# Optimization experiments

Measured on AMD Instinct MI355X. Metric: run time of the kernel, lower is better.

## Reference

```python
import jax, jax.numpy as jnp
import numpy as np

B, T, IN = 8, 1000, 80
CONV = 256
CCEP = 222            # ltv_out_channels
FFT_SIZE = 1024
HOP = 256
WIN = 2 * HOP         # 512
PAD = (FFT_SIZE - CCEP) // 2   # 401
NFFT = 2048


def _conv1d_same(x, W, b, groups):
    # x: (B,T,C); W: (O, C//groups, 3); equivalent to torch Conv1d pad=2 then [1:-1]
    y = jax.lax.conv_general_dilated(
        jnp.transpose(x, (0, 2, 1)), W, (1,), [(1, 1)],
        feature_group_count=groups,
        dimension_numbers=('NCH', 'OIH', 'NCH'))
    return jnp.transpose(y, (0, 2, 1)) + b


def _forward(x, z, W1, b1, W2, b2, W3, b3, W4, b4):
    Bx, Tx, _ = x.shape
    # ---- ConvLayers ----
    h = jax.nn.relu(_conv1d_same(x, W1, b1, 1))
    h = jax.nn.relu(_conv1d_same(h, W2, b2, 8))
    h = jax.nn.relu(_conv1d_same(h, W3, b3, 8))
    ccep = _conv1d_same(h, W4, b4, 1)            # (B,T,222)
    q = jnp.arange(1, CCEP // 2 + 1, dtype=x.dtype)
    quef = jnp.concatenate([q[::-1], q])          # [111..1,1..111]
    ccep = ccep / quef
    # ---- ccep -> impulse (log-magnitude cepstrum -> minimum-ish phase impulse) ----
    c = jnp.pad(ccep, ((0, 0), (0, 0), (PAD, PAD)))           # (B,T,1024)
    Y = jnp.fft.fft(c, n=FFT_SIZE, axis=-1)
    mag = jnp.power(10.0, Y.real)
    imp = jnp.fft.ifft(mag * jnp.exp(1j * Y.imag), n=FFT_SIZE, axis=-1).real  # (B,T,1024)
    # ---- time-varying impulse convolution (cross-correlation per frame) ----
    L = z.shape[-1]
    zz = z.reshape(Bx, 1, L)
    zp = jnp.pad(zz, ((0, 0), (0, 0), (WIN // 2 - 1, WIN // 2)))
    starts = jnp.arange(Tx) * HOP
    frames = zp[:, :, starts[:, None] + jnp.arange(WIN)]       # (B,1,T,512)
    fp = jnp.pad(frames, ((0, 0), (0, 0), (0, 0), (FFT_SIZE // 2 - 1, FFT_SIZE // 2)))  # len 1535
    # corr[s] = sum_k fp[s+k] * imp[k], s in [0,512); linear corr via zero-padded FFT
    Fz = jnp.fft.rfft(fp, n=NFFT, axis=-1)                     # (B,1,T,NFFT//2+1)
    Fy = jnp.fft.rfft(imp, n=NFFT, axis=-1)[:, None]           # (B,1,T,NFFT//2+1)
    corr = jnp.fft.irfft(Fz * jnp.conj(Fy), n=NFFT, axis=-1)[..., :WIN]  # (B,1,T,512)
    # ---- overlap-add ----
    n = jnp.arange(WIN, dtype=x.dtype)
    win = 0.5 * (1.0 - jnp.cos(2.0 * jnp.pi * n / WIN))        # periodic hann, win_norm=1
    zw = corr * win
    l, r = zw[..., :HOP], zw[..., HOP:]
    out = l + jnp.roll(r, 1, axis=2)
    return out.reshape(Bx, 1, Tx * HOP)


def setup_inputs() -> dict:
    key = jax.random.key(0)
    ks = jax.random.split(key, 12)
    x = jax.random.normal(ks[0], (B, T, IN), dtype=jnp.float32)
    z = jax.random.normal(ks[1], (B, 1, T * HOP), dtype=jnp.float32)
    def w(k, o, i, kk, scale):
        return jax.random.normal(k, (o, i, kk), dtype=jnp.float32) * (scale / np.sqrt(i * kk))
    W1 = w(ks[2], CONV, IN, 3, 1.0)
    b1 = jnp.zeros((CONV,), jnp.float32)
    W2 = w(ks[3], CONV, CONV // 8, 3, 1.0)
    b2 = jnp.zeros((CONV,), jnp.float32)
    W3 = w(ks[4], CONV, CONV // 8, 3, 1.0)
    b3 = jnp.zeros((CONV,), jnp.float32)
    W4 = w(ks[5], CCEP, CONV, 3, 0.01)   # small scale keeps 10**(.) well-conditioned
    b4 = jnp.zeros((CCEP,), jnp.float32)
    return {"x": x, "z": z, "W1": W1, "b1": b1, "W2": W2, "b2": b2,
            "W3": W3, "b3": b3, "W4": W4, "b4": b4}


def reference(x, z, W1, b1, W2, b2, W3, b3, W4, b4):
    return _forward(x, z, W1, b1, W2, b2, W3, b3, W4, b4)
```

## Files before the change

kernel.cpp:

```cpp
#include <hip/hip_runtime.h>
#include <hip/hip_bf16.h>

#define T_LEN 1000
#define B_N 8
#define IN_CH 80
#define CONV_CH 256
#define CCEP_N 222

typedef short s8v __attribute__((ext_vector_type(8)));
typedef float f16v __attribute__((ext_vector_type(16)));

#define TWO_PI 6.28318530717958647692f

__global__ __launch_bounds__(256) void k_prep(
    const float* __restrict__ W1, const float* __restrict__ W2,
    const float* __restrict__ W3, const float* __restrict__ W4,
    float* __restrict__ Wt1, float* __restrict__ Wt2, float* __restrict__ Wt3,
    __hip_bfloat16* __restrict__ Wc, float2* __restrict__ twTab,
    float* __restrict__ winTab) {
  const int bid = blockIdx.x, tid = threadIdx.x;
  if (bid < 240) {
    int e = bid * 256 + tid;
    int o = e / 240, k = e - o * 240;
    Wt1[k * 256 + o] = W1[e];
  } else if (bid < 336) {
    int e = (bid - 240) * 256 + tid;
    int o = e / 96, k = e - o * 96;
    Wt2[k * 256 + o] = W2[e];
  } else if (bid < 432) {
    int e = (bid - 336) * 256 + tid;
    int o = e / 96, k = e - o * 96;
    Wt3[k * 256 + o] = W3[e];
  } else if (bid < 1200) {
    int e = (bid - 432) * 256 + tid;
    int kloc = e & 31, n = (e >> 5) & 255, chg = e >> 13;
    int kp = chg * 32 + kloc;
    int kappa = kp >> 8, i = kp & 255;
    float v = 0.f;
    if (n < CCEP_N) {
      float invq = 1.f / (float)((n < 111) ? (111 - n) : (n - 110));
      v = W4[n * 768 + i * 3 + kappa] * invq;
    }
    Wc[e] = __float2bfloat16(v);
  } else {
    int e = (bid - 1200) * 256 + tid;
    if (e < 1020) {
      int Q, off;
      if (e < 768)       { Q = 256; off = 0; }
      else if (e < 960)  { Q = 64;  off = 768; }
      else if (e < 1008) { Q = 16;  off = 960; }
      else               { Q = 4;   off = 1008; }
      int rem = e - off;
      int r = rem / Q, pos = rem - r * Q;
      float ang = (TWO_PI * (float)((r + 1) * pos)) / (float)(4 * Q);
      float s, c;
      sincosf(ang, &s, &c);
      twTab[e] = make_float2(c, s);
    } else if (e < 1532) {
      int n = e - 1020;
      winTab[n] = (0.5f - 0.5f * cosf(TWO_PI * (float)n / 512.f)) * (1.f / 1024.f);
    }
  }
}

__global__ __launch_bounds__(256) void k_conv1t(const float* __restrict__ x,
    const float* __restrict__ Wt, const float* __restrict__ bias,
    float* __restrict__ out) {
  const int b = blockIdx.y;
  const int t0 = blockIdx.x * 10;
  const int o = threadIdx.x;
  __shared__ float hs[IN_CH * 14];
  for (int e = threadIdx.x; e < 12 * IN_CH; e += 256) {
    int r = e / IN_CH, c = e - r * IN_CH;
    int t = t0 - 1 + r;
    hs[c * 14 + r] = (t >= 0 && t < T_LEN) ? x[(b * T_LEN + t) * IN_CH + c] : 0.f;
  }
  __syncthreads();
  float acc[10];
  float bv = bias[o];
#pragma unroll
  for (int j = 0; j < 10; j++) acc[j] = bv;
  for (int i = 0; i < IN_CH; i++) {
    float w0 = Wt[(3 * i + 0) * 256 + o];
    float w1 = Wt[(3 * i + 1) * 256 + o];
    float w2 = Wt[(3 * i + 2) * 256 + o];
    const float* row = &hs[i * 14];
    float a[12];
#pragma unroll
    for (int u = 0; u < 6; u++) *(float2*)&a[2 * u] = *(const float2*)(row + 2 * u);
#pragma unroll
    for (int j = 0; j < 10; j++) {
      acc[j] = fmaf(a[j], w0, acc[j]);
      acc[j] = fmaf(a[j + 1], w1, acc[j]);
      acc[j] = fmaf(a[j + 2], w2, acc[j]);
    }
  }
#pragma unroll
  for (int j = 0; j < 10; j++)
    out[(b * T_LEN + t0 + j) * CONV_CH + o] = fmaxf(acc[j], 0.f);
}

__global__ __launch_bounds__(256) void k_convgt(const float* __restrict__ h,
    const float* __restrict__ Wt, const float* __restrict__ bias,
    float* __restrict__ out) {
  const int b = blockIdx.y;
  const int t0 = blockIdx.x * 10;
  const int o = threadIdx.x;
  const int cb = (o >> 5) << 5;
  __shared__ float hs[CONV_CH * 14];
  for (int e = threadIdx.x; e < 12 * CONV_CH; e += 256) {
    int r = e >> 8, c = e & 255;
    int t = t0 - 1 + r;
    hs[c * 14 + r] = (t >= 0 && t < T_LEN) ? h[(b * T_LEN + t) * CONV_CH + c] : 0.f;
  }
  __syncthreads();
  float acc[10];
  float bv = bias[o];
#pragma unroll
  for (int j = 0; j < 10; j++) acc[j] = bv;
  for (int i = 0; i < 32; i++) {
    float w0 = Wt[(3 * i + 0) * 256 + o];
    float w1 = Wt[(3 * i + 1) * 256 + o];
    float w2 = Wt[(3 * i + 2) * 256 + o];
    const float* row = &hs[(cb + i) * 14];
    float a[12];
#pragma unroll
    for (int u = 0; u < 6; u++) *(float2*)&a[2 * u] = *(const float2*)(row + 2 * u);
#pragma unroll
    for (int j = 0; j < 10; j++) {
      acc[j] = fmaf(a[j], w0, acc[j]);
      acc[j] = fmaf(a[j + 1], w1, acc[j]);
      acc[j] = fmaf(a[j + 2], w2, acc[j]);
    }
  }
#pragma unroll
  for (int j = 0; j < 10; j++)
    out[(b * T_LEN + t0 + j) * CONV_CH + o] = fmaxf(acc[j], 0.f);
}

__global__ __launch_bounds__(256) void k_convgt_b(const float* __restrict__ h,
    const float* __restrict__ Wt, const float* __restrict__ bias,
    __hip_bfloat16* __restrict__ out) {
  const int b = blockIdx.y;
  const int t0 = blockIdx.x * 10;
  const int o = threadIdx.x;
  const int cb = (o >> 5) << 5;
  __shared__ float hs[CONV_CH * 14];
  for (int e = threadIdx.x; e < 12 * CONV_CH; e += 256) {
    int r = e >> 8, c = e & 255;
    int t = t0 - 1 + r;
    hs[c * 14 + r] = (t >= 0 && t < T_LEN) ? h[(b * T_LEN + t) * CONV_CH + c] : 0.f;
  }
  __syncthreads();
  float acc[10];
  float bv = bias[o];
#pragma unroll
  for (int j = 0; j < 10; j++) acc[j] = bv;
  for (int i = 0; i < 32; i++) {
    float w0 = Wt[(3 * i + 0) * 256 + o];
    float w1 = Wt[(3 * i + 1) * 256 + o];
    float w2 = Wt[(3 * i + 2) * 256 + o];
    const float* row = &hs[(cb + i) * 14];
    float a[12];
#pragma unroll
    for (int u = 0; u < 6; u++) *(float2*)&a[2 * u] = *(const float2*)(row + 2 * u);
#pragma unroll
    for (int j = 0; j < 10; j++) {
      acc[j] = fmaf(a[j], w0, acc[j]);
      acc[j] = fmaf(a[j + 1], w1, acc[j]);
      acc[j] = fmaf(a[j + 2], w2, acc[j]);
    }
  }
#pragma unroll
  for (int j = 0; j < 10; j++)
    out[(b * T_LEN + t0 + j) * CONV_CH + o] = __float2bfloat16(fmaxf(acc[j], 0.f));
}

#define APITCH 264
#define BPITCH 40
#define PSTRIDE 1792000
__global__ __launch_bounds__(256) void k_conv4m(
    const __hip_bfloat16* __restrict__ h3, const __hip_bfloat16* __restrict__ Wc,
    const float* __restrict__ bias, float* __restrict__ Pbase) {
  const int mb = blockIdx.x, b = blockIdx.y, ks = blockIdx.z;
  float* __restrict__ P = Pbase + (size_t)ks * PSTRIDE;
  const int t0 = mb * 64;
  const int tid = threadIdx.x;
  const int w = tid >> 6, lane = tid & 63;
  const int wm = w >> 1, wn = w & 1;
  const int lm = lane & 31, half = lane >> 5;

  __shared__ short h3s[67 * APITCH];
  __shared__ short Bs[2][256 * BPITCH];

  const ushort* h3u = (const ushort*)h3;
  for (int g = tid; g < 67 * 64; g += 256) {
    int rr = g >> 6, c4 = g & 63;
    int t = t0 + rr - 1;
    uint2 v = make_uint2(0u, 0u);
    if (t >= 0 && t < T_LEN)
      v = *(const uint2*)(h3u + (b * T_LEN + t) * CONV_CH + c4 * 4);
    *(uint2*)(h3s + rr * APITCH + c4 * 4) = v;
  }

  const ushort* Wu = (const ushort*)(Wc) + (size_t)(ks * 6) * 8192;
#pragma unroll
  for (int it = 0; it < 4; ++it) {
    int idx = (it * 256 + tid) * 8;
    uint4 v = *(const uint4*)(Wu + idx);
    int n = idx >> 5, kloc = idx & 31;
    *(uint4*)(Bs[0] + n * BPITCH + kloc) = v;
  }
  __syncthreads();

  f16v acc0 = {}, acc1 = {}, acc2 = {}, acc3 = {};

  for (int ch = 0; ch < 6; ++ch) {
    const int p = ch & 1;
    if (ch < 5) {
      const ushort* src = Wu + (ch + 1) * 8192;
#pragma unroll
      for (int it = 0; it < 4; ++it) {
        int idx = (it * 256 + tid) * 8;
        uint4 v = *(const uint4*)(src + idx);
        int n = idx >> 5, kloc = idx & 31;
        *(uint4*)(Bs[p ^ 1] + n * BPITCH + kloc) = v;
      }
    }
#pragma unroll
    for (int s = 0; s < 2; ++s) {
      int k0 = ks * 192 + ch * 32 + s * 16;
      int kappa = k0 >> 8, i0 = k0 & 255;
      s8v a = *(const s8v*)(h3s + (wm * 32 + lm + kappa) * APITCH + i0 + half * 8);
      const short* bp = Bs[p] + (wn * 128 + lm) * BPITCH + s * 16 + half * 8;
      s8v b0 = *(const s8v*)(bp);
      s8v b1 = *(const s8v*)(bp + 32 * BPITCH);
      s8v b2 = *(const s8v*)(bp + 64 * BPITCH);
      s8v b3 = *(const s8v*)(bp + 96 * BPITCH);
      acc0 = __builtin_amdgcn_mfma_f32_32x32x16_bf16(a, b0, acc0, 0, 0, 0);
      acc1 = __builtin_amdgcn_mfma_f32_32x32x16_bf16(a, b1, acc1, 0, 0, 0);
      acc2 = __builtin_amdgcn_mfma_f32_32x32x16_bf16(a, b2, acc2, 0, 0, 0);
      acc3 = __builtin_amdgcn_mfma_f32_32x32x16_bf16(a, b3, acc3, 0, 0, 0);
    }
    __syncthreads();
  }

  const int col = lm;
#pragma unroll
  for (int nt = 0; nt < 4; ++nt) {
    int c = wn * 128 + nt * 32 + col;
    if (c >= CCEP_N) continue;
    float bq = 0.f;
    if (ks == 0) {
      float invq = 1.f / (float)((c < 111) ? (111 - c) : (c - 110));
      bq = bias[c] * invq;
    }
    const f16v* A = (nt == 0) ? &acc0 : (nt == 1) ? &acc1 : (nt == 2) ? &acc2 : &acc3;
#pragma unroll
    for (int reg = 0; reg < 16; ++reg) {
      int row = (reg & 3) + 8 * (reg >> 2) + 4 * half;
      int t = t0 + wm * 32 + row;
      if (t < T_LEN)
        P[(size_t)(b * T_LEN + t) * 224 + c] = (*A)[reg] + bq;
    }
  }
}

__device__ __forceinline__ float2 cmul(float2 a, float2 b) {
  return make_float2(fmaf(a.x, b.x, -(a.y * b.y)), fmaf(a.x, b.y, a.y * b.x));
}
__device__ __forceinline__ float2 cadd(float2 a, float2 b) { return make_float2(a.x + b.x, a.y + b.y); }
__device__ __forceinline__ float2 csub(float2 a, float2 b) { return make_float2(a.x - b.x, a.y - b.y); }

#define LIDX(i) ((i) + ((i) >> 2))

template <int Q, int OFF>
__device__ __forceinline__ void fwd_stage_t(float2* __restrict__ X,
    const float2* __restrict__ Tw, int j) {
  const int pos = j & (Q - 1);
  const int base = ((j - pos) << 2) + pos;
  float2 e1 = Tw[OFF + pos], e2 = Tw[OFF + Q + pos], e3 = Tw[OFF + 2 * Q + pos];
  const float2 w1 = make_float2(e1.x, -e1.y);
  const float2 w2 = make_float2(e2.x, -e2.y);
  const float2 w3 = make_float2(e3.x, -e3.y);
  float2 a = X[LIDX(base)], b = X[LIDX(base + Q)];
  float2 cc = X[LIDX(base + 2 * Q)], d = X[LIDX(base + 3 * Q)];
  float2 t0 = cadd(a, cc), t1 = csub(a, cc), t2 = cadd(b, d), bd = csub(b, d);
  float2 t3 = make_float2(bd.y, -bd.x);
  X[LIDX(base)]         = cadd(t0, t2);
  X[LIDX(base + Q)]     = cmul(cadd(t1, t3), w1);
  X[LIDX(base + 2 * Q)] = cmul(csub(t0, t2), w2);
  X[LIDX(base + 3 * Q)] = cmul(csub(t1, t3), w3);
}

template <int Q, int OFF>
__device__ __forceinline__ void inv_stage_t(float2* __restrict__ X,
    const float2* __restrict__ Tw, int j) {
  const int pos = j & (Q - 1);
  const int base = ((j - pos) << 2) + pos;
  const float2 w1 = Tw[OFF + pos];
  const float2 w2 = Tw[OFF + Q + pos];
  const float2 w3 = Tw[OFF + 2 * Q + pos];
  float2 a = X[LIDX(base)];
  float2 b = cmul(X[LIDX(base + Q)], w1);
  float2 cc = cmul(X[LIDX(base + 2 * Q)], w2);
  float2 d = cmul(X[LIDX(base + 3 * Q)], w3);
  float2 t0 = cadd(a, cc), t1 = csub(a, cc), t2 = cadd(b, d), bd = csub(b, d);
  float2 t3 = make_float2(-bd.y, bd.x);
  X[LIDX(base)]         = cadd(t0, t2);
  X[LIDX(base + Q)]     = cadd(t1, t3);
  X[LIDX(base + 2 * Q)] = csub(t0, t2);
  X[LIDX(base + 3 * Q)] = csub(t1, t3);
}

__device__ __forceinline__ int rev4d(int v) {
  return ((v & 3) << 6) | (((v >> 2) & 3) << 4) | (((v >> 4) & 3) << 2) | ((v >> 6) & 3);
}

__global__ __launch_bounds__(256) void k_fft(const float* __restrict__ Pb,
    const float* __restrict__ z, const float2* __restrict__ twg,
    const float* __restrict__ wing, float* __restrict__ out) {
  const int t = blockIdx.x, b = blockIdx.y;
  const int bt = b * T_LEN + t;
  const int j = threadIdx.x;
  __shared__ float2 Wl[1280];
  __shared__ float2 Tws[1020];
  for (int e = j; e < 1020; e += 256) Tws[e] = twg[e];

  const float* zb = z + b * 256000;
  float f0 = 0.f, f1 = 0.f, c1 = 0.f, c2 = 0.f;
  {
    int zi0 = t * 256 + j - 255;
    if (zi0 >= 0) f0 = zb[zi0];
    int zi1 = t * 256 + j + 1;
    if (zi1 < 256000) f1 = zb[zi1];
    if (j >= 145) {
      int m = bt * 224 + (j - 145);
      c1 = (Pb[m] + Pb[m + PSTRIDE]) + (Pb[m + 2 * PSTRIDE] + Pb[m + 3 * PSTRIDE]);
    }
    if (j < 111) {
      int m = bt * 224 + (j + 111);
      c2 = (Pb[m] + Pb[m + PSTRIDE]) + (Pb[m + 2 * PSTRIDE] + Pb[m + 3 * PSTRIDE]);
    }
  }
  __syncthreads();

  {
    float2 e1 = Tws[j], e2 = Tws[256 + j], e3 = Tws[512 + j];
    const float2 w1 = make_float2(e1.x, -e1.y);
    const float2 w2 = make_float2(e2.x, -e2.y);
    const float2 w3 = make_float2(e3.x, -e3.y);
    float2 t0 = make_float2(c2, f0);
    float2 t1 = make_float2(-c2, f0);
    float2 t2 = make_float2(c1, f1);
    float2 t3 = make_float2(f1, -c1);
    Wl[LIDX(j)]       = cadd(t0, t2);
    Wl[LIDX(j + 256)] = cmul(cadd(t1, t3), w1);
    Wl[LIDX(j + 512)] = cmul(csub(t0, t2), w2);
    Wl[LIDX(j + 768)] = cmul(csub(t1, t3), w3);
  }
  __syncthreads();

  fwd_stage_t<64, 768>(Wl, Tws, j);  __syncthreads();
  fwd_stage_t<16, 960>(Wl, Tws, j);  __syncthreads();
  fwd_stage_t<4, 1008>(Wl, Tws, j);  __syncthreads();

  const int base = 4 * j;
  float2 X[4];
  {
    float2 u0 = Wl[LIDX(base)], u1 = Wl[LIDX(base + 1)];
    float2 u2 = Wl[LIDX(base + 2)], u3 = Wl[LIDX(base + 3)];
    float2 t0 = cadd(u0, u2), t1 = csub(u0, u2), t2 = cadd(u1, u3), bd = csub(u1, u3);
    float2 t3 = make_float2(bd.y, -bd.x);
    X[0] = cadd(t0, t2); X[1] = cadd(t1, t3); X[2] = csub(t0, t2); X[3] = csub(t1, t3);
  }
#pragma unroll
  for (int q = 0; q < 4; ++q) Wl[LIDX(base + q)] = X[q];
  __syncthreads();

  const int r0 = rev4d(j);
  const bool self0 = (r0 == 0);
  const int jp = self0 ? 0 : rev4d((256 - r0) & 255);
  float2 P[4];
#pragma unroll
  for (int q = 0; q < 4; ++q) P[q] = Wl[LIDX(4 * jp + q)];
  float2 S[4];
#pragma unroll
  for (int q = 0; q < 4; ++q) {
    float2 A = X[q];
    float2 Bc0 = P[(4 - q) & 3];
    float2 Bc1 = P[3 - q];
    float2 Bc = self0 ? Bc0 : Bc1;
    float2 Y = make_float2(0.5f * (A.x + Bc.x), 0.5f * (A.y - Bc.y));
    float2 F = make_float2(0.5f * (A.y + Bc.y), -0.5f * (A.x - Bc.x));
    float mag = __expf(Y.x * 2.30258509299404568402f);
    float sy, cy;
    __sincosf(Y.y, &sy, &cy);
    float gr = mag * cy, gi = mag * sy;
    S[q] = make_float2(fmaf(F.x, gr, F.y * gi), fmaf(F.x, gi, -(F.y * gr)));
  }
  __syncthreads();
  {
    float2 t0 = cadd(S[0], S[2]), t1 = csub(S[0], S[2]), t2 = cadd(S[1], S[3]), bd = csub(S[1], S[3]);
    float2 t3 = make_float2(-bd.y, bd.x);
    Wl[LIDX(base)]     = cadd(t0, t2);
    Wl[LIDX(base + 1)] = cadd(t1, t3);
    Wl[LIDX(base + 2)] = csub(t0, t2);
    Wl[LIDX(base + 3)] = csub(t1, t3);
  }
  __syncthreads();

  inv_stage_t<4, 1008>(Wl, Tws, j);  __syncthreads();
  inv_stage_t<16, 960>(Wl, Tws, j);  __syncthreads();
  inv_stage_t<64, 768>(Wl, Tws, j);  __syncthreads();

  {
    float2 w1 = Tws[j], w2 = Tws[256 + j], w3 = Tws[512 + j];
    float2 A = Wl[LIDX(j)];
    float2 B = Wl[LIDX(j + 256)];
    float2 C2 = Wl[LIDX(j + 512)];
    float2 D = Wl[LIDX(j + 768)];
    float bx = fmaf(B.x, w1.x, -(B.y * w1.y)), by = fmaf(B.x, w1.y, B.y * w1.x);
    float cx = fmaf(C2.x, w2.x, -(C2.y * w2.y));
    float dx = fmaf(D.x, w3.x, -(D.y * w3.y)), dy = fmaf(D.x, w3.y, D.y * w3.x);
    float cj    = (A.x + cx) + (bx + dx);
    float cj256 = (A.x - cx) - (by - dy);
    int n1 = 511 - j, n2 = 255 - j;
    float wn1 = wing[n1], wn2 = wing[n2];
    int tp = (t + 1 == T_LEN) ? 0 : t + 1;
    atomicAdd(&out[b * 256000 + t * 256 + n2], cj256 * wn2);
    atomicAdd(&out[b * 256000 + tp * 256 + n2], cj * wn1);
  }
}

extern "C" void kernel_launch(void* const* d_in, const int* in_sizes, int n_in,
                              void* d_out, int out_size, void* d_ws, size_t ws_size,
                              hipStream_t stream) {
  const float* x  = (const float*)d_in[0];
  const float* z  = (const float*)d_in[1];
  const float* W1 = (const float*)d_in[2];
  const float* b1 = (const float*)d_in[3];
  const float* W2 = (const float*)d_in[4];
  const float* b2 = (const float*)d_in[5];
  const float* W3 = (const float*)d_in[6];
  const float* b3 = (const float*)d_in[7];
  const float* W4 = (const float*)d_in[8];
  const float* b4 = (const float*)d_in[9];

  float* ws   = (float*)d_ws;
  float* bufA = ws;
  float* bufC = ws + 2048000;
  __hip_bfloat16* h3bf = (__hip_bfloat16*)(ws + 4096000);
  float* Pb   = ws + 5120000;
  float* Wt1  = ws + 12288000;
  float* Wt2  = ws + 12349440;
  float* Wt3  = ws + 12374016;
  __hip_bfloat16* Wc = (__hip_bfloat16*)(ws + 12398592);
  float2* twTab = (float2*)(ws + 12496896);
  float* winTab = ws + 12498944;

  float* out = (float*)d_out;
  hipMemsetAsync(out, 0, (size_t)2048000 * sizeof(float), stream);

  dim3 blk(256);
  k_prep<<<1206, blk, 0, stream>>>(W1, W2, W3, W4, Wt1, Wt2, Wt3, Wc, twTab, winTab);

  dim3 cgrid10(T_LEN / 10, B_N);
  k_conv1t<<<cgrid10, blk, 0, stream>>>(x, Wt1, b1, bufA);
  k_convgt<<<cgrid10, blk, 0, stream>>>(bufA, Wt2, b2, bufC);
  k_convgt_b<<<cgrid10, blk, 0, stream>>>(bufC, Wt3, b3, h3bf);
  dim3 g4(16, B_N, 4);
  k_conv4m<<<g4, blk, 0, stream>>>(h3bf, Wc, b4, Pb);
  dim3 gf(T_LEN, B_N);
  k_fft<<<gf, blk, 0, stream>>>(Pb, z, twTab, winTab, out);
}
```

Before: 179.5 us.

## Fuse grouped convs, pack two frames per FFT, fold output zeroing into prep

Three separate changes. First, the output memset moves into the prep kernel as extra blocks. Second, the two grouped conv layers are fused into one kernel that keeps the intermediate activations in shared memory, at the cost of recomputing halo rows. Third, the FFT kernel handles two adjacent frames per block: it packs both real inverse transforms into one complex IFFT and shares the overlapping z samples, which halves the inverse FFT work and cuts the number of atomics. The trade-off is more shared memory and registers per block, and half as many blocks.

```diff
diff --git a/kernel.cpp b/kernel.cpp
--- a/kernel.cpp
+++ b/kernel.cpp
@@ -17,7 +17,7 @@
     const float* __restrict__ W3, const float* __restrict__ W4,
     float* __restrict__ Wt1, float* __restrict__ Wt2, float* __restrict__ Wt3,
     __hip_bfloat16* __restrict__ Wc, float2* __restrict__ twTab,
-    float* __restrict__ winTab) {
+    float* __restrict__ winTab, float* __restrict__ out) {
   const int bid = blockIdx.x, tid = threadIdx.x;
   if (bid < 240) {
     int e = bid * 256 + tid;
@@ -42,7 +42,7 @@
       v = W4[n * 768 + i * 3 + kappa] * invq;
     }
     Wc[e] = __float2bfloat16(v);
-  } else {
+  } else if (bid < 1206) {
     int e = (bid - 1200) * 256 + tid;
     if (e < 1020) {
       int Q, off;
@@ -60,6 +60,11 @@
       int n = e - 1020;
       winTab[n] = (0.5f - 0.5f * cosf(TWO_PI * (float)n / 512.f)) * (1.f / 1024.f);
     }
+  } else {
+    int e = ((bid - 1206) * 256 + tid) * 8;
+    float4 zz = make_float4(0.f, 0.f, 0.f, 0.f);
+    *(float4*)(out + e) = zz;
+    *(float4*)(out + e + 4) = zz;
   }
 }
 
@@ -100,80 +105,73 @@
     out[(b * T_LEN + t0 + j) * CONV_CH + o] = fmaxf(acc[j], 0.f);
 }
 
-__global__ __launch_bounds__(256) void k_convgt(const float* __restrict__ h,
-    const float* __restrict__ Wt, const float* __restrict__ bias,
-    float* __restrict__ out) {
-  const int b = blockIdx.y;
-  const int t0 = blockIdx.x * 10;
-  const int o = threadIdx.x;
-  const int cb = (o >> 5) << 5;
-  __shared__ float hs[CONV_CH * 14];
-  for (int e = threadIdx.x; e < 12 * CONV_CH; e += 256) {
-    int r = e >> 8, c = e & 255;
-    int t = t0 - 1 + r;
-    hs[c * 14 + r] = (t >= 0 && t < T_LEN) ? h[(b * T_LEN + t) * CONV_CH + c] : 0.f;
-  }
-  __syncthreads();
-  float acc[10];
-  float bv = bias[o];
-#pragma unroll
-  for (int j = 0; j < 10; j++) acc[j] = bv;
-  for (int i = 0; i < 32; i++) {
-    float w0 = Wt[(3 * i + 0) * 256 + o];
-    float w1 = Wt[(3 * i + 1) * 256 + o];
-    float w2 = Wt[(3 * i + 2) * 256 + o];
-    const float* row = &hs[(cb + i) * 14];
-    float a[12];
-#pragma unroll
-    for (int u = 0; u < 6; u++) *(float2*)&a[2 * u] = *(const float2*)(row + 2 * u);
-#pragma unroll
-    for (int j = 0; j < 10; j++) {
-      acc[j] = fmaf(a[j], w0, acc[j]);
-      acc[j] = fmaf(a[j + 1], w1, acc[j]);
-      acc[j] = fmaf(a[j + 2], w2, acc[j]);
-    }
-  }
-#pragma unroll
-  for (int j = 0; j < 10; j++)
-    out[(b * T_LEN + t0 + j) * CONV_CH + o] = fmaxf(acc[j], 0.f);
-}
-
-__global__ __launch_bounds__(256) void k_convgt_b(const float* __restrict__ h,
-    const float* __restrict__ Wt, const float* __restrict__ bias,
+__global__ __launch_bounds__(256) void k_convg2(const float* __restrict__ h,
+    const float* __restrict__ Wt2, const float* __restrict__ b2,
+    const float* __restrict__ Wt3, const float* __restrict__ b3,
     __hip_bfloat16* __restrict__ out) {
   const int b = blockIdx.y;
   const int t0 = blockIdx.x * 10;
   const int o = threadIdx.x;
   const int cb = (o >> 5) << 5;
-  __shared__ float hs[CONV_CH * 14];
-  for (int e = threadIdx.x; e < 12 * CONV_CH; e += 256) {
+  __shared__ float hs1[CONV_CH * 14];
+  __shared__ float hs2[CONV_CH * 14];
+  for (int e = threadIdx.x; e < 14 * CONV_CH; e += 256) {
     int r = e >> 8, c = e & 255;
-    int t = t0 - 1 + r;
-    hs[c * 14 + r] = (t >= 0 && t < T_LEN) ? h[(b * T_LEN + t) * CONV_CH + c] : 0.f;
-  }
-  __syncthreads();
-  float acc[10];
-  float bv = bias[o];
-#pragma unroll
-  for (int j = 0; j < 10; j++) acc[j] = bv;
-  for (int i = 0; i < 32; i++) {
-    float w0 = Wt[(3 * i + 0) * 256 + o];
-    float w1 = Wt[(3 * i + 1) * 256 + o];
-    float w2 = Wt[(3 * i + 2) * 256 + o];
-    const float* row = &hs[(cb + i) * 14];
-    float a[12];
-#pragma unroll
-    for (int u = 0; u < 6; u++) *(float2*)&a[2 * u] = *(const float2*)(row + 2 * u);
-#pragma unroll
-    for (int j = 0; j < 10; j++) {
-      acc[j] = fmaf(a[j], w0, acc[j]);
-      acc[j] = fmaf(a[j + 1], w1, acc[j]);
-      acc[j] = fmaf(a[j + 2], w2, acc[j]);
-    }
-  }
-#pragma unroll
-  for (int j = 0; j < 10; j++)
-    out[(b * T_LEN + t0 + j) * CONV_CH + o] = __float2bfloat16(fmaxf(acc[j], 0.f));
+    int t = t0 - 2 + r;
+    hs1[c * 14 + r] = (t >= 0 && t < T_LEN) ? h[(b * T_LEN + t) * CONV_CH + c] : 0.f;
+  }
+  __syncthreads();
+  {
+    float acc[12];
+    float bv = b2[o];
+#pragma unroll
+    for (int j = 0; j < 12; j++) acc[j] = bv;
+    for (int i = 0; i < 32; i++) {
+      float w0 = Wt2[(3 * i + 0) * 256 + o];
+      float w1 = Wt2[(3 * i + 1) * 256 + o];
+      float w2 = Wt2[(3 * i + 2) * 256 + o];
+      const float* row = &hs1[(cb + i) * 14];
+      float a[14];
+#pragma unroll
+      for (int u = 0; u < 7; u++) *(float2*)&a[2 * u] = *(const float2*)(row + 2 * u);
+#pragma unroll
+      for (int j = 0; j < 12; j++) {
+        acc[j] = fmaf(a[j], w0, acc[j]);
+        acc[j] = fmaf(a[j + 1], w1, acc[j]);
+        acc[j] = fmaf(a[j + 2], w2, acc[j]);
+      }
+    }
+#pragma unroll
+    for (int j = 0; j < 12; j++) {
+      int t = t0 - 1 + j;
+      hs2[o * 14 + j] = (t >= 0 && t < T_LEN) ? fmaxf(acc[j], 0.f) : 0.f;
+    }
+  }
+  __syncthreads();
+  {
+    float acc[10];
+    float bv = b3[o];
+#pragma unroll
+    for (int j = 0; j < 10; j++) acc[j] = bv;
+    for (int i = 0; i < 32; i++) {
+      float w0 = Wt3[(3 * i + 0) * 256 + o];
+      float w1 = Wt3[(3 * i + 1) * 256 + o];
+      float w2 = Wt3[(3 * i + 2) * 256 + o];
+      const float* row = &hs2[(cb + i) * 14];
+      float a[12];
+#pragma unroll
+      for (int u = 0; u < 6; u++) *(float2*)&a[2 * u] = *(const float2*)(row + 2 * u);
+#pragma unroll
+      for (int j = 0; j < 10; j++) {
+        acc[j] = fmaf(a[j], w0, acc[j]);
+        acc[j] = fmaf(a[j + 1], w1, acc[j]);
+        acc[j] = fmaf(a[j + 2], w2, acc[j]);
+      }
+    }
+#pragma unroll
+    for (int j = 0; j < 10; j++)
+      out[(b * T_LEN + t0 + j) * CONV_CH + o] = __float2bfloat16(fmaxf(acc[j], 0.f));
+  }
 }
 
 #define APITCH 264
@@ -275,22 +273,26 @@
 #define LIDX(i) ((i) + ((i) >> 2))
 
 template <int Q, int OFF>
-__device__ __forceinline__ void fwd_stage_t(float2* __restrict__ X,
-    const float2* __restrict__ Tw, int j) {
+__device__ __forceinline__ void fwd_stage2(float2* __restrict__ A,
+    float2* __restrict__ B, const float2* __restrict__ Tw, int j) {
   const int pos = j & (Q - 1);
   const int base = ((j - pos) << 2) + pos;
   float2 e1 = Tw[OFF + pos], e2 = Tw[OFF + Q + pos], e3 = Tw[OFF + 2 * Q + pos];
   const float2 w1 = make_float2(e1.x, -e1.y);
   const float2 w2 = make_float2(e2.x, -e2.y);
   const float2 w3 = make_float2(e3.x, -e3.y);
-  float2 a = X[LIDX(base)], b = X[LIDX(base + Q)];
-  float2 cc = X[LIDX(base + 2 * Q)], d = X[LIDX(base + 3 * Q)];
-  float2 t0 = cadd(a, cc), t1 = csub(a, cc), t2 = cadd(b, d), bd = csub(b, d);
-  float2 t3 = make_float2(bd.y, -bd.x);
-  X[LIDX(base)]         = cadd(t0, t2);
-  X[LIDX(base + Q)]     = cmul(cadd(t1, t3), w1);
-  X[LIDX(base + 2 * Q)] = cmul(csub(t0, t2), w2);
-  X[LIDX(base + 3 * Q)] = cmul(csub(t1, t3), w3);
+#pragma unroll
+  for (int arr = 0; arr < 2; ++arr) {
+    float2* X = arr ? B : A;
+    float2 a = X[LIDX(base)], b = X[LIDX(base + Q)];
+    float2 cc = X[LIDX(base + 2 * Q)], d = X[LIDX(base + 3 * Q)];
+    float2 t0 = cadd(a, cc), t1 = csub(a, cc), t2 = cadd(b, d), bd = csub(b, d);
+    float2 t3 = make_float2(bd.y, -bd.x);
+    X[LIDX(base)]         = cadd(t0, t2);
+    X[LIDX(base + Q)]     = cmul(cadd(t1, t3), w1);
+    X[LIDX(base + 2 * Q)] = cmul(csub(t0, t2), w2);
+    X[LIDX(base + 3 * Q)] = cmul(csub(t1, t3), w3);
+  }
 }
 
 template <int Q, int OFF>
@@ -320,28 +322,34 @@
 __global__ __launch_bounds__(256) void k_fft(const float* __restrict__ Pb,
     const float* __restrict__ z, const float2* __restrict__ twg,
     const float* __restrict__ wing, float* __restrict__ out) {
-  const int t = blockIdx.x, b = blockIdx.y;
-  const int bt = b * T_LEN + t;
+  const int u = blockIdx.x, b = blockIdx.y;
+  const int tA = 2 * u, tB = tA + 1;
+  const int btA = b * T_LEN + tA, btB = btA + 1;
   const int j = threadIdx.x;
-  __shared__ float2 Wl[1280];
+  __shared__ float2 WlA[1280];
+  __shared__ float2 WlB[1280];
   __shared__ float2 Tws[1020];
   for (int e = j; e < 1020; e += 256) Tws[e] = twg[e];
 
   const float* zb = z + b * 256000;
-  float f0 = 0.f, f1 = 0.f, c1 = 0.f, c2 = 0.f;
-  {
-    int zi0 = t * 256 + j - 255;
-    if (zi0 >= 0) f0 = zb[zi0];
-    int zi1 = t * 256 + j + 1;
-    if (zi1 < 256000) f1 = zb[zi1];
-    if (j >= 145) {
-      int m = bt * 224 + (j - 145);
-      c1 = (Pb[m] + Pb[m + PSTRIDE]) + (Pb[m + 2 * PSTRIDE] + Pb[m + 3 * PSTRIDE]);
-    }
-    if (j < 111) {
-      int m = bt * 224 + (j + 111);
-      c2 = (Pb[m] + Pb[m + PSTRIDE]) + (Pb[m + 2 * PSTRIDE] + Pb[m + 3 * PSTRIDE]);
-    }
+  float f0A = 0.f, fS, f1B = 0.f;
+  {
+    int zi0 = tA * 256 + j - 255;
+    f0A = (zi0 >= 0) ? zb[zi0] : 0.f;
+    fS = zb[tA * 256 + j + 1];
+    int zi2 = tB * 256 + j + 1;
+    f1B = (zi2 < 256000) ? zb[zi2] : 0.f;
+  }
+  float c1A = 0.f, c2A = 0.f, c1B = 0.f, c2B = 0.f;
+  if (j >= 145) {
+    int mA = btA * 224 + (j - 145), mB = btB * 224 + (j - 145);
+    c1A = (Pb[mA] + Pb[mA + PSTRIDE]) + (Pb[mA + 2 * PSTRIDE] + Pb[mA + 3 * PSTRIDE]);
+    c1B = (Pb[mB] + Pb[mB + PSTRIDE]) + (Pb[mB + 2 * PSTRIDE] + Pb[mB + 3 * PSTRIDE]);
+  }
+  if (j < 111) {
+    int mA = btA * 224 + (j + 111), mB = btB * 224 + (j + 111);
+    c2A = (Pb[mA] + Pb[mA + PSTRIDE]) + (Pb[mA + 2 * PSTRIDE] + Pb[mA + 3 * PSTRIDE]);
+    c2B = (Pb[mB] + Pb[mB + PSTRIDE]) + (Pb[mB + 2 * PSTRIDE] + Pb[mB + 3 * PSTRIDE]);
   }
   __syncthreads();
 
@@ -350,86 +358,123 @@
     const float2 w1 = make_float2(e1.x, -e1.y);
     const float2 w2 = make_float2(e2.x, -e2.y);
     const float2 w3 = make_float2(e3.x, -e3.y);
-    float2 t0 = make_float2(c2, f0);
-    float2 t1 = make_float2(-c2, f0);
-    float2 t2 = make_float2(c1, f1);
-    float2 t3 = make_float2(f1, -c1);
-    Wl[LIDX(j)]       = cadd(t0, t2);
-    Wl[LIDX(j + 256)] = cmul(cadd(t1, t3), w1);
-    Wl[LIDX(j + 512)] = cmul(csub(t0, t2), w2);
-    Wl[LIDX(j + 768)] = cmul(csub(t1, t3), w3);
-  }
-  __syncthreads();
-
-  fwd_stage_t<64, 768>(Wl, Tws, j);  __syncthreads();
-  fwd_stage_t<16, 960>(Wl, Tws, j);  __syncthreads();
-  fwd_stage_t<4, 1008>(Wl, Tws, j);  __syncthreads();
+    {
+      float2 t0 = make_float2(c2A, f0A);
+      float2 t1 = make_float2(-c2A, f0A);
+      float2 t2 = make_float2(c1A, fS);
+      float2 t3 = make_float2(fS, -c1A);
+      WlA[LIDX(j)]       = cadd(t0, t2);
+      WlA[LIDX(j + 256)] = cmul(cadd(t1, t3), w1);
+      WlA[LIDX(j + 512)] = cmul(csub(t0, t2), w2);
+      WlA[LIDX(j + 768)] = cmul(csub(t1, t3), w3);
+    }
+    {
+      float2 t0 = make_float2(c2B, fS);
+      float2 t1 = make_float2(-c2B, fS);
+      float2 t2 = make_float2(c1B, f1B);
+      float2 t3 = make_float2(f1B, -c1B);
+      WlB[LIDX(j)]       = cadd(t0, t2);
+      WlB[LIDX(j + 256)] = cmul(cadd(t1, t3), w1);
+      WlB[LIDX(j + 512)] = cmul(csub(t0, t2), w2);
+      WlB[LIDX(j + 768)] = cmul(csub(t1, t3), w3);
+    }
+  }
+  __syncthreads();
+
+  fwd_stage2<64, 768>(WlA, WlB, Tws, j);  __syncthreads();
+  fwd_stage2<16, 960>(WlA, WlB, Tws, j);  __syncthreads();
+  fwd_stage2<4, 1008>(WlA, WlB, Tws, j);  __syncthreads();
 
   const int base = 4 * j;
-  float2 X[4];
-  {
-    float2 u0 = Wl[LIDX(base)], u1 = Wl[LIDX(base + 1)];
-    float2 u2 = Wl[LIDX(base + 2)], u3 = Wl[LIDX(base + 3)];
+  float2 XA[4], XB[4];
+  {
+    float2 u0 = WlA[LIDX(base)], u1 = WlA[LIDX(base + 1)];
+    float2 u2 = WlA[LIDX(base + 2)], u3 = WlA[LIDX(base + 3)];
     float2 t0 = cadd(u0, u2), t1 = csub(u0, u2), t2 = cadd(u1, u3), bd = csub(u1, u3);
     float2 t3 = make_float2(bd.y, -bd.x);
-    X[0] = cadd(t0, t2); X[1] = cadd(t1, t3); X[2] = csub(t0, t2); X[3] = csub(t1, t3);
-  }
-#pragma unroll
-  for (int q = 0; q < 4; ++q) Wl[LIDX(base + q)] = X[q];
+    XA[0] = cadd(t0, t2); XA[1] = cadd(t1, t3); XA[2] = csub(t0, t2); XA[3] = csub(t1, t3);
+  }
+  {
+    float2 u0 = WlB[LIDX(base)], u1 = WlB[LIDX(base + 1)];
+    float2 u2 = WlB[LIDX(base + 2)], u3 = WlB[LIDX(base + 3)];
+    float2 t0 = cadd(u0, u2), t1 = csub(u0, u2), t2 = cadd(u1, u3), bd = csub(u1, u3);
+    float2 t3 = make_float2(bd.y, -bd.x);
+    XB[0] = cadd(t0, t2); XB[1] = cadd(t1, t3); XB[2] = csub(t0, t2); XB[3] = csub(t1, t3);
+  }
+#pragma unroll
+  for (int q = 0; q < 4; ++q) { WlA[LIDX(base + q)] = XA[q]; WlB[LIDX(base + q)] = XB[q]; }
   __syncthreads();
 
   const int r0 = rev4d(j);
   const bool self0 = (r0 == 0);
   const int jp = self0 ? 0 : rev4d((256 - r0) & 255);
-  float2 P[4];
-#pragma unroll
-  for (int q = 0; q < 4; ++q) P[q] = Wl[LIDX(4 * jp + q)];
-  float2 S[4];
+  float2 PA[4], PB[4];
+#pragma unroll
+  for (int q = 0; q < 4; ++q) { PA[q] = WlA[LIDX(4 * jp + q)]; PB[q] = WlB[LIDX(4 * jp + q)]; }
+  float2 Z[4];
 #pragma unroll
   for (int q = 0; q < 4; ++q) {
-    float2 A = X[q];
-    float2 Bc0 = P[(4 - q) & 3];
-    float2 Bc1 = P[3 - q];
-    float2 Bc = self0 ? Bc0 : Bc1;
-    float2 Y = make_float2(0.5f * (A.x + Bc.x), 0.5f * (A.y - Bc.y));
-    float2 F = make_float2(0.5f * (A.y + Bc.y), -0.5f * (A.x - Bc.x));
-    float mag = __expf(Y.x * 2.30258509299404568402f);
-    float sy, cy;
-    __sincosf(Y.y, &sy, &cy);
-    float gr = mag * cy, gi = mag * sy;
-    S[q] = make_float2(fmaf(F.x, gr, F.y * gi), fmaf(F.x, gi, -(F.y * gr)));
-  }
-  __syncthreads();
-  {
-    float2 t0 = cadd(S[0], S[2]), t1 = csub(S[0], S[2]), t2 = cadd(S[1], S[3]), bd = csub(S[1], S[3]);
+    float2 SA, SB;
+    {
+      float2 A = XA[q];
+      float2 Bc = self0 ? PA[(4 - q) & 3] : PA[3 - q];
+      float2 Y = make_float2(0.5f * (A.x + Bc.x), 0.5f * (A.y - Bc.y));
+      float2 F = make_float2(0.5f * (A.y + Bc.y), -0.5f * (A.x - Bc.x));
+      float mag = __expf(Y.x * 2.30258509299404568402f);
+      float sy, cy;
+      __sincosf(Y.y, &sy, &cy);
+      float gr = mag * cy, gi = mag * sy;
+      SA = make_float2(fmaf(F.x, gr, F.y * gi), fmaf(F.x, gi, -(F.y * gr)));
+    }
+    {
+      float2 A = XB[q];
+      float2 Bc = self0 ? PB[(4 - q) & 3] : PB[3 - q];
+      float2 Y = make_float2(0.5f * (A.x + Bc.x), 0.5f * (A.y - Bc.y));
+      float2 F = make_float2(0.5f * (A.y + Bc.y), -0.5f * (A.x - Bc.x));
+      float mag = __expf(Y.x * 2.30258509299404568402f);
+      float sy, cy;
+      __sincosf(Y.y, &sy, &cy);
+      float gr = mag * cy, gi = mag * sy;
+      SB = make_float2(fmaf(F.x, gr, F.y * gi), fmaf(F.x, gi, -(F.y * gr)));
+    }
+    Z[q] = make_float2(SA.x - SB.y, SA.y + SB.x);
+  }
+  __syncthreads();
+
+  {
+    float2 t0 = cadd(Z[0], Z[2]), t1 = csub(Z[0], Z[2]), t2 = cadd(Z[1], Z[3]), bd = csub(Z[1], Z[3]);
     float2 t3 = make_float2(-bd.y, bd.x);
-    Wl[LIDX(base)]     = cadd(t0, t2);
-    Wl[LIDX(base + 1)] = cadd(t1, t3);
-    Wl[LIDX(base + 2)] = csub(t0, t2);
-    Wl[LIDX(base + 3)] = csub(t1, t3);
-  }
-  __syncthreads();
-
-  inv_stage_t<4, 1008>(Wl, Tws, j);  __syncthreads();
-  inv_stage_t<16, 960>(Wl, Tws, j);  __syncthreads();
-  inv_stage_t<64, 768>(Wl, Tws, j);  __syncthreads();
+    WlA[LIDX(base)]     = cadd(t0, t2);
+    WlA[LIDX(base + 1)] = cadd(t1, t3);
+    WlA[LIDX(base + 2)] = csub(t0, t2);
+    WlA[LIDX(base + 3)] = csub(t1, t3);
+  }
+  __syncthreads();
+
+  inv_stage_t<4, 1008>(WlA, Tws, j);  __syncthreads();
+  inv_stage_t<16, 960>(WlA, Tws, j);  __syncthreads();
+  inv_stage_t<64, 768>(WlA, Tws, j);  __syncthreads();
 
   {
     float2 w1 = Tws[j], w2 = Tws[256 + j], w3 = Tws[512 + j];
-    float2 A = Wl[LIDX(j)];
-    float2 B = Wl[LIDX(j + 256)];
-    float2 C2 = Wl[LIDX(j + 512)];
-    float2 D = Wl[LIDX(j + 768)];
-    float bx = fmaf(B.x, w1.x, -(B.y * w1.y)), by = fmaf(B.x, w1.y, B.y * w1.x);
-    float cx = fmaf(C2.x, w2.x, -(C2.y * w2.y));
-    float dx = fmaf(D.x, w3.x, -(D.y * w3.y)), dy = fmaf(D.x, w3.y, D.y * w3.x);
-    float cj    = (A.x + cx) + (bx + dx);
-    float cj256 = (A.x - cx) - (by - dy);
+    float2 a = WlA[LIDX(j)];
+    float2 bb = cmul(WlA[LIDX(j + 256)], w1);
+    float2 cc = cmul(WlA[LIDX(j + 512)], w2);
+    float2 d = cmul(WlA[LIDX(j + 768)], w3);
+    float2 t0 = cadd(a, cc), t1 = csub(a, cc), t2 = cadd(bb, d), bd = csub(bb, d);
+    float2 t3 = make_float2(-bd.y, bd.x);
+    float2 Cj    = cadd(t0, t2);
+    float2 Cj256 = cadd(t1, t3);
     int n1 = 511 - j, n2 = 255 - j;
     float wn1 = wing[n1], wn2 = wing[n2];
-    int tp = (t + 1 == T_LEN) ? 0 : t + 1;
-    atomicAdd(&out[b * 256000 + t * 256 + n2], cj256 * wn2);
-    atomicAdd(&out[b * 256000 + tp * 256 + n2], cj * wn1);
+    float vA_l = Cj256.x * wn2;
+    float vAB  = Cj.x * wn1 + Cj256.y * wn2;
+    float vB_r = Cj.y * wn1;
+    int tw = (tB + 1 == T_LEN) ? 0 : tB + 1;
+    float* ob = out + b * 256000;
+    atomicAdd(&ob[tA * 256 + n2], vA_l);
+    atomicAdd(&ob[tB * 256 + n2], vAB);
+    atomicAdd(&ob[tw * 256 + n2], vB_r);
   }
 }
 
@@ -449,28 +494,25 @@
 
   float* ws   = (float*)d_ws;
   float* bufA = ws;
-  float* bufC = ws + 2048000;
-  __hip_bfloat16* h3bf = (__hip_bfloat16*)(ws + 4096000);
-  float* Pb   = ws + 5120000;
-  float* Wt1  = ws + 12288000;
-  float* Wt2  = ws + 12349440;
-  float* Wt3  = ws + 12374016;
-  __hip_bfloat16* Wc = (__hip_bfloat16*)(ws + 12398592);
-  float2* twTab = (float2*)(ws + 12496896);
-  float* winTab = ws + 12498944;
-
+  __hip_bfloat16* h3bf = (__hip_bfloat16*)(ws + 2048000);
+  float* Pb   = ws + 3072000;
+  float* Wt1  = ws + 10240000;
+  float* Wt2  = ws + 10301440;
+  float* Wt3  = ws + 10326016;
+  __hip_bfloat16* Wc = (__hip_bfloat16*)(ws + 10350592);
+  float2* twTab = (float2*)(ws + 10448896);
+  float* winTab = ws + 10450944;
   float* out = (float*)d_out;
-  hipMemsetAsync(out, 0, (size_t)2048000 * sizeof(float), stream);
 
   dim3 blk(256);
-  k_prep<<<1206, blk, 0, stream>>>(W1, W2, W3, W4, Wt1, Wt2, Wt3, Wc, twTab, winTab);
+  k_prep<<<2206, blk, 0, stream>>>(W1, W2, W3, W4, Wt1, Wt2, Wt3, Wc,
+                                   twTab, winTab, out);
 
   dim3 cgrid10(T_LEN / 10, B_N);
   k_conv1t<<<cgrid10, blk, 0, stream>>>(x, Wt1, b1, bufA);
-  k_convgt<<<cgrid10, blk, 0, stream>>>(bufA, Wt2, b2, bufC);
-  k_convgt_b<<<cgrid10, blk, 0, stream>>>(bufC, Wt3, b3, h3bf);
+  k_convg2<<<cgrid10, blk, 0, stream>>>(bufA, Wt2, b2, Wt3, b3, h3bf);
   dim3 g4(16, B_N, 4);
   k_conv4m<<<g4, blk, 0, stream>>>(h3bf, Wc, b4, Pb);
-  dim3 gf(T_LEN, B_N);
+  dim3 gf(T_LEN / 2, B_N);
   k_fft<<<gf, blk, 0, stream>>>(Pb, z, twTab, winTab, out);
 }
```

Result: faster. 172.6 us (-3.9%).
